# Kernel optimization log

Measured on AMD Instinct MI355X. Metric: run time of the kernel, lower is better.

## Reference

```python
import jax, jax.numpy as jnp
import numpy as np

H, HKV, D, HIDDEN = 32, 8, 128, 4096
G = H // HKV  # GQA group size = 4
ROPE_THETA = 10000.0


def fwht(x):
    """Fast Walsh-Hadamard transform over the last axis (scale=1, like faster_hadamard_transform default)."""
    d = x.shape[-1]
    orig = x.shape
    x = x.reshape(-1, d)
    h = 1
    while h < d:
        x = x.reshape(-1, d // (2 * h), 2, h)
        a, b = x[:, :, 0, :], x[:, :, 1, :]
        x = jnp.stack([a + b, a - b], axis=2).reshape(-1, d)
        h *= 2
    return x.reshape(orig)


def rope(x, pos):
    """NeoX-style (rotate-half) RoPE at scalar position `pos`; x: [..., D]."""
    half = D // 2
    inv_freq = 1.0 / (ROPE_THETA ** (jnp.arange(0, D, 2, dtype=jnp.float32) / D))  # [half]
    ang = jnp.float32(pos) * inv_freq
    cos, sin = jnp.cos(ang), jnp.sin(ang)
    x1, x2 = x[..., :half], x[..., half:]
    return jnp.concatenate([x1 * cos - x2 * sin, x2 * cos + x1 * sin], axis=-1)


def quant2bit(x):
    """2-bit quantization of Hadamard-domain vectors: per-vector scale = mean(|x|), codes in {-2,-1,0,1}."""
    s = jnp.mean(jnp.abs(x), axis=-1, keepdims=True) + 1e-6
    code = jnp.clip(jnp.round(x / s), -2.0, 1.0)
    return code, s


def _forward(hidden_states, Wq, Wk, Wv, Wo, k_cache, v_cache, top_k):
    x = hidden_states[0, 0]                                 # [HIDDEN]
    q = (x @ Wq.T).reshape(H, D)
    k = (x @ Wk.T).reshape(HKV, D)
    v = (x @ Wv.T).reshape(HKV, D)
    pos = k_cache.shape[0]                                  # decode position (cache len before append)
    q = rope(q, pos)
    k = rope(k, pos)
    # append to cache -> total T = S + 1 tokens
    K = jnp.concatenate([k_cache, k[None]], axis=0)          # [T, HKV, D]
    V = jnp.concatenate([v_cache, v[None]], axis=0)          # [T, HKV, D]
    T = K.shape[0]
    # Hadamard transform + 2-bit codes for estimation
    hq = fwht(q)                                             # [H, D]
    hK = fwht(K)                                             # [T, HKV, D]
    cq, sq = quant2bit(hq)                                   # [H,D], [H,1]
    ck, sk = quant2bit(hK)                                   # [T,HKV,D], [T,HKV,1]
    # estimated attention scores from low-bit codes, per query head
    est = jnp.einsum('ngd,tnd->ngt', cq.reshape(HKV, G, D), ck).reshape(H, T)
    skh = jnp.repeat(sk[:, :, 0].T, G, axis=0)               # [H, T]
    est = est * sq * skh
    est = est.at[:, -1].set(jnp.inf)                         # always keep the current token
    # top-k index selection per head
    _, idx = jax.lax.top_k(est, top_k)                       # [H, top_k]
    kv_map = jnp.arange(H) // G                              # [H]
    Ksel = K[idx, kv_map[:, None], :]                        # [H, top_k, D]
    Vsel = V[idx, kv_map[:, None], :]                        # [H, top_k, D]
    # sparse attention over selected tokens
    logits = jnp.einsum('hd,hkd->hk', q, Ksel) / jnp.sqrt(jnp.float32(D))
    p = jax.nn.softmax(logits, axis=-1)
    attn = jnp.einsum('hk,hkd->hd', p, Vsel).reshape(HIDDEN)
    return (attn @ Wo.T).reshape(1, 1, HIDDEN)


def setup_inputs() -> dict:
    key = jax.random.key(0)
    ks = jax.random.split(key, 7)
    S = 32767
    w = 1.0 / np.sqrt(HIDDEN)
    return {
        'hidden_states': jax.random.normal(ks[0], (1, 1, HIDDEN), jnp.float32),
        'Wq': jax.random.normal(ks[1], (H * D, HIDDEN), jnp.float32) * w,
        'Wk': jax.random.normal(ks[2], (HKV * D, HIDDEN), jnp.float32) * w,
        'Wv': jax.random.normal(ks[3], (HKV * D, HIDDEN), jnp.float32) * w,
        'Wo': jax.random.normal(ks[4], (HIDDEN, HIDDEN), jnp.float32) * w,
        'k_cache': jax.random.normal(ks[5], (S, HKV, D), jnp.float32),
        'v_cache': jax.random.normal(ks[6], (S, HKV, D), jnp.float32),
        'top_k': 2048,
    }


def reference(hidden_states, Wq, Wk, Wv, Wo, k_cache, v_cache, top_k):
    return _forward(hidden_states, Wq, Wk, Wv, Wo, k_cache, v_cache, top_k)
```

## Files before the change

kernel.cpp:

```cpp
#include <hip/hip_runtime.h>
#include <math.h>


#if defined(__has_builtin)
#if __has_builtin(__builtin_amdgcn_sdot4)
#define HAVE_SDOT4 1
#endif
#endif

__device__ __forceinline__ int dot4(int a, int b, int c) {
#ifdef HAVE_SDOT4
  return __builtin_amdgcn_sdot4(a, b, c, false);
#else
  return c + ((a << 24) >> 24) * ((b << 24) >> 24) +
         (((a << 16) >> 24)) * (((b << 16) >> 24)) +
         (((a << 8) >> 24)) * (((b << 8) >> 24)) + (a >> 24) * (b >> 24);
#endif
}

__device__ __forceinline__ unsigned enc_f32(float f) {
  unsigned u = __float_as_uint(f);
  return (u & 0x80000000u) ? ~u : (u | 0x80000000u);
}

__global__ __launch_bounds__(256) void k_gemv_qkv(
    const float* __restrict__ x, const float* __restrict__ Wq,
    const float* __restrict__ Wk, const float* __restrict__ Wv,
    float* __restrict__ y, unsigned* __restrict__ gz) {
  if (blockIdx.x < 96) {
    const int base = blockIdx.x * 512 + threadIdx.x;
    ((uint4*)gz)[base] = make_uint4(0u, 0u, 0u, 0u);
    ((uint4*)gz)[base + 256] = make_uint4(0u, 0u, 0u, 0u);
  }
  const int lane = threadIdx.x & 63;
  const int wid = threadIdx.x >> 6;
  const int row = blockIdx.x * 4 + wid;
  const float* W;
  if (row < 4096) W = Wq + (size_t)row * 4096;
  else if (row < 5120) W = Wk + (size_t)(row - 4096) * 4096;
  else W = Wv + (size_t)(row - 5120) * 4096;
  const float4* W4 = (const float4*)W;
  const float4* x4 = (const float4*)x;
  float acc = 0.f;
#pragma unroll
  for (int i = 0; i < 16; ++i) {
    float4 w = W4[i * 64 + lane];
    float4 xv = x4[i * 64 + lane];
    acc = fmaf(w.x, xv.x, acc);
    acc = fmaf(w.y, xv.y, acc);
    acc = fmaf(w.z, xv.z, acc);
    acc = fmaf(w.w, xv.w, acc);
  }
#pragma unroll
  for (int off = 32; off >= 1; off >>= 1) acc += __shfl_xor(acc, off);
  if (lane == 0) y[row] = acc;
}

__global__ __launch_bounds__(64) void k_rope_quant(
    const float* __restrict__ y, float* __restrict__ q_rope,
    float* __restrict__ k_rope, signed char* __restrict__ cq_i8,
    float* __restrict__ sq, int pos) {
  const int h = blockIdx.x;
  const int lane = threadIdx.x;
  const float* row = (h < 32) ? (y + (size_t)h * 128)
                              : (y + 4096 + (size_t)(h - 32) * 128);
  float x1 = row[lane];
  float x2 = row[lane + 64];
  double e = (double)lane / 64.0;
  float pf = (float)pow(10000.0, e);
  float invf = 1.0f / pf;
  float ang = (float)pos * invf;
  float c = (float)cos((double)ang);
  float s = (float)sin((double)ang);
  float r1 = __fsub_rn(__fmul_rn(x1, c), __fmul_rn(x2, s));
  float r2 = __fadd_rn(__fmul_rn(x2, c), __fmul_rn(x1, s));
  if (h >= 32) {
    k_rope[(size_t)(h - 32) * 128 + lane] = r1;
    k_rope[(size_t)(h - 32) * 128 + 64 + lane] = r2;
    return;
  }
  q_rope[(size_t)h * 128 + lane] = r1;
  q_rope[(size_t)h * 128 + 64 + lane] = r2;
  float a = r1, b = r2;
#pragma unroll
  for (int m = 1; m <= 32; m <<= 1) {
    float ta = __shfl_xor(a, m), tb = __shfl_xor(b, m);
    bool up = (lane & m) == 0;
    a = up ? (a + ta) : (ta - a);
    b = up ? (b + tb) : (tb - b);
  }
  { float na = a + b, nb = a - b; a = na; b = nb; }
  float asum = fabsf(a) + fabsf(b);
#pragma unroll
  for (int m = 32; m >= 1; m >>= 1) asum += __shfl_xor(asum, m);
  float sc = asum * (1.0f / 128.0f) + 1e-6f;
  float ca = fminf(fmaxf(rintf(a / sc), -2.0f), 1.0f);
  float cb = fminf(fmaxf(rintf(b / sc), -2.0f), 1.0f);
  cq_i8[(size_t)h * 128 + lane] = (signed char)(int)ca;
  cq_i8[(size_t)h * 128 + 64 + lane] = (signed char)(int)cb;
  if (lane == 0) sq[h] = sc;
}

__global__ __launch_bounds__(64, 1) void k_quant_est(
    const float* __restrict__ kc, const signed char* __restrict__ cq_i8,
    const float* __restrict__ sq, unsigned* __restrict__ ekeys, int S, int T) {
  const int lane = threadIdx.x;
  const int n = blockIdx.y;
  const int t = blockIdx.x * 64 + lane;
  const bool act = t < S;
  const float4* src = (const float4*)(kc + ((size_t)(act ? t : 0) * 8 + n) * 128);
  float f[128];
#pragma unroll
  for (int j = 0; j < 32; ++j) {
    float4 v = src[j];
    f[4 * j + 0] = v.x; f[4 * j + 1] = v.y; f[4 * j + 2] = v.z; f[4 * j + 3] = v.w;
  }
#pragma unroll
  for (int hh = 1; hh < 128; hh <<= 1) {
#pragma unroll
    for (int i = 0; i < 128; i += 2 * hh) {
#pragma unroll
      for (int k = 0; k < hh; ++k) {
        float a = f[i + k], b = f[i + hh + k];
        f[i + k] = a + b;
        f[i + hh + k] = a - b;
      }
    }
  }
  float s0 = 0.f, s1 = 0.f, s2 = 0.f, s3 = 0.f;
#pragma unroll
  for (int j = 0; j < 32; ++j) {
    s0 += fabsf(f[4 * j + 0]); s1 += fabsf(f[4 * j + 1]);
    s2 += fabsf(f[4 * j + 2]); s3 += fabsf(f[4 * j + 3]);
  }
  const float sc = ((s0 + s1) + (s2 + s3)) * (1.0f / 128.0f) + 1e-6f;
  unsigned pw[32];
#pragma unroll
  for (int w = 0; w < 32; ++w) {
    unsigned word = 0;
#pragma unroll
    for (int j = 0; j < 4; ++j) {
      float cf = fminf(fmaxf(rintf(f[4 * w + j] / sc), -2.0f), 1.0f);
      int ci = (int)cf;
      word |= ((unsigned)(ci & 255)) << (8 * j);
    }
    pw[w] = word;
  }
  int acc0 = 0, acc1 = 0, acc2 = 0, acc3 = 0;
  const int* cqw = (const int*)cq_i8;
#pragma unroll
  for (int w = 0; w < 32; ++w) {
    int ck = (int)pw[w];
    acc0 = dot4(ck, cqw[(n * 4 + 0) * 32 + w], acc0);
    acc1 = dot4(ck, cqw[(n * 4 + 1) * 32 + w], acc1);
    acc2 = dot4(ck, cqw[(n * 4 + 2) * 32 + w], acc2);
    acc3 = dot4(ck, cqw[(n * 4 + 3) * 32 + w], acc3);
  }
  int accs[4] = {acc0, acc1, acc2, acc3};
#pragma unroll
  for (int g = 0; g < 4; ++g) {
    float v = ((float)accs[g] * sq[n * 4 + g]) * sc;
    unsigned key = act ? enc_f32(v) : 0xFF800000u;
    ekeys[(size_t)(n * 4 + g) * T + t] = key;
  }
}

template <int NB>
__device__ __forceinline__ void radix_scan(const unsigned* __restrict__ hrow,
                                           unsigned need_in, unsigned& bsel,
                                           unsigned& need_out) {
  const int lane = threadIdx.x & 63;
  constexpr int PL = NB / 64;
  unsigned b[PL];
  unsigned s = 0u;
  const uint4* bp = (const uint4*)(hrow + lane * PL);
#pragma unroll
  for (int i = 0; i < PL / 4; ++i) {
    uint4 v = bp[i];
    b[4 * i] = v.x; b[4 * i + 1] = v.y; b[4 * i + 2] = v.z; b[4 * i + 3] = v.w;
    s += v.x + v.y + v.z + v.w;
  }
  unsigned inc = s;
#pragma unroll
  for (int off = 1; off < 64; off <<= 1) {
    unsigned tv = __shfl_down(inc, off);
    if (lane + off < 64) inc += tv;
  }
  const unsigned suf = inc - s;
  const bool win = (suf < need_in) && (suf + s >= need_in);
  unsigned bs = 0u, n2 = 0u;
  if (win) {
    unsigned running = suf;
#pragma unroll
    for (int i = PL - 1; i >= 0; --i) {
      unsigned cb = b[i];
      if (running + cb >= need_in) { bs = (unsigned)(lane * PL + i); n2 = need_in - running; break; }
      running += cb;
    }
  }
  unsigned long long mw = __ballot(win);
  int srcl = (int)__builtin_ctzll(mw);
  bsel = __shfl(bs, srcl);
  need_out = __shfl(n2, srcl);
}

__global__ __launch_bounds__(256) void k_hist(
    const unsigned* __restrict__ keys, const unsigned* __restrict__ g0,
    const unsigned* __restrict__ g1, unsigned* __restrict__ gout,
    const int* __restrict__ topk_ptr, int pass, int T) {
  const int h = blockIdx.y, c = blockIdx.x, tid = threadIdx.x;
  __shared__ unsigned lh[2048];
#pragma unroll
  for (int i = 0; i < 8; ++i) lh[tid + 256 * i] = 0u;

  int shift, pshift; unsigned mask;
  if (pass == 0) { shift = 21; mask = 0x7FFu; pshift = 0; }
  else if (pass == 1) { shift = 10; mask = 0x7FFu; pshift = 21; }
  else { shift = 0; mask = 0x3FFu; pshift = 10; }

  unsigned pref = 0u;
  if (pass >= 1) {
    const unsigned K = (unsigned)(*topk_ptr);
    unsigned b, nd;
    radix_scan<2048>(g0 + h * 2048, K, b, nd);
    pref = b;
    if (pass == 2) {
      unsigned b1, n1;
      radix_scan<2048>(g1 + h * 2048, nd, b1, n1);
      pref = (pref << 11) | b1;
    }
  }
  __syncthreads();
  const uint4* row = (const uint4*)(keys + (size_t)h * T + c * 2048);
#pragma unroll
  for (int j = 0; j < 2; ++j) {
    uint4 v = row[tid * 2 + j];
    unsigned u[4] = {v.x, v.y, v.z, v.w};
#pragma unroll
    for (int e = 0; e < 4; ++e) {
      bool ok = (pass == 0) || ((u[e] >> pshift) == pref);
      if (ok) atomicAdd(&lh[(u[e] >> shift) & mask], 1u);
    }
  }
  __syncthreads();
#pragma unroll
  for (int i = 0; i < 8; ++i) {
    unsigned cnt = lh[tid + 256 * i];
    if (cnt) atomicAdd(&gout[h * 2048 + tid + 256 * i], cnt);
  }
}

__global__ __launch_bounds__(256) void k_compact(
    const unsigned* __restrict__ keys, const unsigned* __restrict__ g0,
    const unsigned* __restrict__ g1, const unsigned* __restrict__ g2,
    int* __restrict__ idx_out, const int* __restrict__ topk_ptr, int T) {
  const int h = blockIdx.y, c = blockIdx.x, tid = threadIdx.x;
  const unsigned K = (unsigned)(*topk_ptr);
  unsigned b, need, thr;
  radix_scan<2048>(g0 + h * 2048, K, b, need);
  thr = b;
  radix_scan<2048>(g1 + h * 2048, need, b, need);
  thr = (thr << 11) | b;
  radix_scan<1024>(g2 + h * 2048, need, b, need);
  thr = (thr << 10) | b;
  const unsigned gt_total = K - need;

  const unsigned* rowbase = keys + (size_t)h * T;
  unsigned cg = 0u, ce = 0u;
  for (int i = 0; i < c; ++i) {
    const uint4* ch = (const uint4*)(rowbase + i * 2048);
#pragma unroll
    for (int j = 0; j < 2; ++j) {
      uint4 v = ch[tid * 2 + j];
      cg += (v.x > thr) + (v.y > thr) + (v.z > thr) + (v.w > thr);
      ce += (v.x == thr) + (v.y == thr) + (v.z == thr) + (v.w == thr);
    }
  }
  unsigned red = (cg << 16) | ce;
#pragma unroll
  for (int off = 32; off >= 1; off >>= 1) red += __shfl_xor(red, off);
  __shared__ unsigned wsum[4];
  __shared__ unsigned scn[256];
  if ((tid & 63) == 0) wsum[tid >> 6] = red;
  __syncthreads();
  const unsigned basep = wsum[0] + wsum[1] + wsum[2] + wsum[3];
  const unsigned bg = basep >> 16, be = basep & 0xFFFFu;

  const uint4* row = (const uint4*)(rowbase + c * 2048);
  unsigned u[8];
  {
    uint4 v0 = row[tid * 2], v1 = row[tid * 2 + 1];
    u[0] = v0.x; u[1] = v0.y; u[2] = v0.z; u[3] = v0.w;
    u[4] = v1.x; u[5] = v1.y; u[6] = v1.z; u[7] = v1.w;
  }
  unsigned mcg = 0u, mce = 0u;
#pragma unroll
  for (int e = 0; e < 8; ++e) { mcg += (u[e] > thr); mce += (u[e] == thr); }
  unsigned packed = (mcg << 16) | mce;
  scn[tid] = packed;
  __syncthreads();
#pragma unroll
  for (int off = 1; off < 256; off <<= 1) {
    unsigned v = (tid >= off) ? scn[tid - off] : 0u;
    __syncthreads();
    scn[tid] += v;
    __syncthreads();
  }
  const unsigned excl = scn[tid] - packed;
  unsigned exg = bg + (excl >> 16);
  unsigned exe = be + (excl & 0xFFFFu);
  const unsigned tb = (unsigned)(c * 2048 + tid * 8);
  int* dst = idx_out + (size_t)h * K;
#pragma unroll
  for (int e = 0; e < 8; ++e) {
    if (u[e] > thr) dst[exg++] = (int)(tb + e);
    else if (u[e] == thr) {
      unsigned r = exe++;
      if (r < need) dst[gt_total + r] = (int)(tb + e);
    }
  }
}

#define SPLITS 64
#define PSTR 132
__global__ __launch_bounds__(256) void k_attn(
    const float* __restrict__ kc, const float* __restrict__ vc,
    const float* __restrict__ k_rope, const float* __restrict__ v_new,
    const float* __restrict__ q_rope, const int* __restrict__ idx,
    const int* __restrict__ topk_ptr, float* __restrict__ part, int S) {
  const int lane = threadIdx.x & 63;
  const int wid = threadIdx.x >> 6;
  const int h = blockIdx.x;
  const int split = blockIdx.y;
  const int K = *topk_ptr;
  const int n = h >> 2;
  const int per_block = (K + SPLITS - 1) / SPLITS;
  const int j0 = split * per_block;
  const int j1 = min(K, j0 + per_block);
  const int per_wave = (per_block + 3) >> 2;
  const int base = j0 + wid * per_wave;
  float2 qv = ((const float2*)(q_rope + (size_t)h * 128))[lane];
  float ssum = 0.f, a0 = 0.f, a1 = 0.f;
  const float scl = 0.08838834764831845f;
  for (int b = 0; b < per_wave; b += 4) {
    float2 kk[4], vv[4];
    bool val[4];
#pragma unroll
    for (int u = 0; u < 4; ++u) {
      const int j = base + b + u;
      val[u] = (j < j1) && (base + b + u >= j0);
      int t = val[u] ? idx[(size_t)h * (size_t)K + j] : 0;
      const float* kr = (t < S) ? (kc + ((size_t)t * 8 + n) * 128)
                                : (k_rope + (size_t)n * 128);
      const float* vr = (t < S) ? (vc + ((size_t)t * 8 + n) * 128)
                                : (v_new + (size_t)n * 128);
      kk[u] = ((const float2*)kr)[lane];
      vv[u] = ((const float2*)vr)[lane];
    }
    float d[4];
#pragma unroll
    for (int u = 0; u < 4; ++u) d[u] = fmaf(qv.x, kk[u].x, qv.y * kk[u].y);
#pragma unroll
    for (int mm = 32; mm >= 1; mm >>= 1) {
#pragma unroll
      for (int u = 0; u < 4; ++u) d[u] += __shfl_xor(d[u], mm);
    }
#pragma unroll
    for (int u = 0; u < 4; ++u) {
      float p = val[u] ? expf(d[u] * scl) : 0.f;
      ssum += p;
      a0 = fmaf(p, vv[u].x, a0);
      a1 = fmaf(p, vv[u].y, a1);
    }
  }
  __shared__ float lds[4][129];
  lds[wid][2 * lane] = a0;
  lds[wid][2 * lane + 1] = a1;
  if (lane == 0) lds[wid][128] = ssum;
  __syncthreads();
  float* pp = part + (size_t)(h * SPLITS + split) * PSTR;
  const int tid = threadIdx.x;
  if (tid < 128) {
    float s = lds[0][tid] + lds[1][tid] + lds[2][tid] + lds[3][tid];
    pp[1 + tid] = s;
  } else if (tid == 128) {
    pp[0] = lds[0][128] + lds[1][128] + lds[2][128] + lds[3][128];
  }
}

__global__ __launch_bounds__(128) void k_combine(const float* __restrict__ part,
                                                 float* __restrict__ attn) {
  const int h = blockIdx.x;
  const int tid = threadIdx.x;
  const float* base = part + (size_t)h * SPLITS * PSTR;
  float acc = 0.f, ssum = 0.f;
  for (int s = 0; s < SPLITS; ++s) {
    const float* pp = base + (size_t)s * PSTR;
    acc += pp[1 + tid];
    ssum += pp[0];
  }
  attn[(size_t)h * 128 + tid] = acc / ssum;
}

__global__ __launch_bounds__(256) void k_gemv_out(
    const float* __restrict__ attn, const float* __restrict__ Wo,
    float* __restrict__ out) {
  const int lane = threadIdx.x & 63;
  const int wid = threadIdx.x >> 6;
  const int row = blockIdx.x * 4 + wid;
  const float4* W4 = (const float4*)(Wo + (size_t)row * 4096);
  const float4* x4 = (const float4*)attn;
  float acc = 0.f;
#pragma unroll
  for (int i = 0; i < 16; ++i) {
    float4 w = W4[i * 64 + lane];
    float4 xv = x4[i * 64 + lane];
    acc = fmaf(w.x, xv.x, acc);
    acc = fmaf(w.y, xv.y, acc);
    acc = fmaf(w.z, xv.z, acc);
    acc = fmaf(w.w, xv.w, acc);
  }
#pragma unroll
  for (int off = 32; off >= 1; off >>= 1) acc += __shfl_xor(acc, off);
  if (lane == 0) out[row] = acc;
}

extern "C" void kernel_launch(void* const* d_in, const int* in_sizes, int n_in,
                              void* d_out, int out_size, void* d_ws, size_t ws_size,
                              hipStream_t stream) {
  const float* x  = (const float*)d_in[0];
  const float* Wq = (const float*)d_in[1];
  const float* Wk = (const float*)d_in[2];
  const float* Wv = (const float*)d_in[3];
  const float* Wo = (const float*)d_in[4];
  const float* kc = (const float*)d_in[5];
  const float* vc = (const float*)d_in[6];
  const int* topk_ptr = (const int*)d_in[7];
  const int S = in_sizes[5] / (8 * 128);
  const int T = S + 1;

  float* ws = (float*)d_ws;
  float* y      = ws + 0;
  float* q_rope = ws + 6144;
  float* k_rope = ws + 10240;
  float* sq     = ws + 11264;
  float* attn   = ws + 11328;
  signed char* cq_i8 = (signed char*)(ws + 15424);
  unsigned* ekeys = (unsigned*)(ws + 16448);
  unsigned* ghist = (unsigned*)(ws + 1065024);
  unsigned* g0 = ghist, *g1 = ghist + 65536, *g2 = ghist + 131072;
  int*   idx    = (int*)(ws + 1261632);
  float* part   = ws + 1523776;

  const int chunks = T / 2048;

  k_gemv_qkv<<<1536, 256, 0, stream>>>(x, Wq, Wk, Wv, y, ghist);
  k_rope_quant<<<40, 64, 0, stream>>>(y, q_rope, k_rope, cq_i8, sq, S);
  k_quant_est<<<dim3(T / 64, 8), 64, 0, stream>>>(kc, cq_i8, sq, ekeys, S, T);

  k_hist<<<dim3(chunks, 32), 256, 0, stream>>>(ekeys, g0, g1, g0, topk_ptr, 0, T);
  k_hist<<<dim3(chunks, 32), 256, 0, stream>>>(ekeys, g0, g1, g1, topk_ptr, 1, T);
  k_hist<<<dim3(chunks, 32), 256, 0, stream>>>(ekeys, g0, g1, g2, topk_ptr, 2, T);
  k_compact<<<dim3(chunks, 32), 256, 0, stream>>>(ekeys, g0, g1, g2, idx, topk_ptr, T);

  k_attn<<<dim3(32, SPLITS), 256, 0, stream>>>(kc, vc, k_rope, y + 5120, q_rope,
                                               idx, topk_ptr, part, S);
  k_combine<<<32, 128, 0, stream>>>(part, attn);
  k_gemv_out<<<1024, 256, 0, stream>>>(attn, Wo, (float*)d_out);
}
```

Before: 116.9 us.

## Stage K-cache rows through swizzled LDS tile for coalesced loads in quant_est

The quantize-and-estimate kernel used to have each lane read its own 512-byte K row with strided float4 loads. Each 64-lane block now loads a contiguous 32KB slab (64 rows covering 8 tokens by 8 KV heads) with fully coalesced float4 reads. It stores the slab into shared memory with a rotation swizzle to avoid bank conflicts, and each lane then reads its row from LDS. The grid is flattened so each lane's head and token come from the lane index, and a bounds guard is added on the key writes. The cost is 32KB of LDS per block, which may limit occupancy, plus an extra sync and LDS round-trip; the ekeys writes also become more scattered across heads.

```diff
diff --git a/kernel.cpp b/kernel.cpp
--- a/kernel.cpp
+++ b/kernel.cpp
@@ -104,15 +104,27 @@
 __global__ __launch_bounds__(64, 1) void k_quant_est(
     const float* __restrict__ kc, const signed char* __restrict__ cq_i8,
     const float* __restrict__ sq, unsigned* __restrict__ ekeys, int S, int T) {
-  const int lane = threadIdx.x;
-  const int n = blockIdx.y;
-  const int t = blockIdx.x * 64 + lane;
-  const bool act = t < S;
-  const float4* src = (const float4*)(kc + ((size_t)(act ? t : 0) * 8 + n) * 128);
+  __shared__ float tile[8192];
+  const int l = threadIdx.x;
+  const int R = S * 8;
+  const size_t base4 = (size_t)blockIdx.x * 2048;
+  const float4* kc4 = (const float4*)kc;
+  float4* tile4 = (float4*)tile;
+#pragma unroll
+  for (int i = 0; i < 32; ++i) {
+    const int F = i * 64 + l;
+    const int row = F >> 5;
+    const int c = F & 31;
+    const long gr = (long)blockIdx.x * 64 + row;
+    const size_t gidx = (gr < R) ? (base4 + (size_t)F) : (size_t)c;
+    float4 v = kc4[gidx];
+    tile4[row * 32 + ((c + row) & 31)] = v;
+  }
+  __syncthreads();
   float f[128];
 #pragma unroll
   for (int j = 0; j < 32; ++j) {
-    float4 v = src[j];
+    float4 v = tile4[l * 32 + ((j + l) & 31)];
     f[4 * j + 0] = v.x; f[4 * j + 1] = v.y; f[4 * j + 2] = v.z; f[4 * j + 3] = v.w;
   }
 #pragma unroll
@@ -146,6 +158,7 @@
     }
     pw[w] = word;
   }
+  const int n = l & 7;
   int acc0 = 0, acc1 = 0, acc2 = 0, acc3 = 0;
   const int* cqw = (const int*)cq_i8;
 #pragma unroll
@@ -156,12 +169,16 @@
     acc2 = dot4(ck, cqw[(n * 4 + 2) * 32 + w], acc2);
     acc3 = dot4(ck, cqw[(n * 4 + 3) * 32 + w], acc3);
   }
+  const int t = blockIdx.x * 8 + (l >> 3);
+  const bool act = t < S;
   int accs[4] = {acc0, acc1, acc2, acc3};
-#pragma unroll
-  for (int g = 0; g < 4; ++g) {
-    float v = ((float)accs[g] * sq[n * 4 + g]) * sc;
-    unsigned key = act ? enc_f32(v) : 0xFF800000u;
-    ekeys[(size_t)(n * 4 + g) * T + t] = key;
+  if (t < T) {
+#pragma unroll
+    for (int g = 0; g < 4; ++g) {
+      float v = ((float)accs[g] * sq[n * 4 + g]) * sc;
+      unsigned key = act ? enc_f32(v) : 0xFF800000u;
+      ekeys[(size_t)(n * 4 + g) * T + t] = key;
+    }
   }
 }
 
@@ -453,10 +470,11 @@
   float* part   = ws + 1523776;
 
   const int chunks = T / 2048;
+  const int nblk = (8 * S + 8 + 63) / 64;
 
   k_gemv_qkv<<<1536, 256, 0, stream>>>(x, Wq, Wk, Wv, y, ghist);
   k_rope_quant<<<40, 64, 0, stream>>>(y, q_rope, k_rope, cq_i8, sq, S);
-  k_quant_est<<<dim3(T / 64, 8), 64, 0, stream>>>(kc, cq_i8, sq, ekeys, S, T);
+  k_quant_est<<<nblk, 64, 0, stream>>>(kc, cq_i8, sq, ekeys, S, T);
 
   k_hist<<<dim3(chunks, 32), 256, 0, stream>>>(ekeys, g0, g1, g0, topk_ptr, 0, T);
   k_hist<<<dim3(chunks, 32), 256, 0, stream>>>(ekeys, g0, g1, g1, topk_ptr, 1, T);
```

Result: slower. 141.6 us (+21.2%).

## Remap quant-estimate threads to contiguous cache rows and vectorize Hadamard butterflies

Applied to the files above, without the earlier changes.

The quant/estimate kernel now assigns one thread per flattened (token, kv-head) row, so each 64-thread block reads one contiguous stretch of the K cache instead of rows strided across heads. The 128-point Walsh-Hadamard transform is rewritten as explicit float4-vector butterflies. Quantization is fused directly into the int8 dot-product loop, removing the packed-code array and easing register pressure. In exchange, score-key writes become less coalesced, because neighbouring lanes now write to eight different head rows.

```diff
diff --git a/kernel.cpp b/kernel.cpp
--- a/kernel.cpp
+++ b/kernel.cpp
@@ -1,6 +1,8 @@
 #include <hip/hip_runtime.h>
 #include <math.h>
 
+
+typedef __attribute__((ext_vector_type(4))) float f32x4;
 
 #if defined(__has_builtin)
 #if __has_builtin(__builtin_amdgcn_sdot4)
@@ -101,67 +103,78 @@
   if (lane == 0) sq[h] = sc;
 }
 
+#define REP32(M) M(0) M(1) M(2) M(3) M(4) M(5) M(6) M(7) M(8) M(9) M(10) M(11) \
+  M(12) M(13) M(14) M(15) M(16) M(17) M(18) M(19) M(20) M(21) M(22) M(23) \
+  M(24) M(25) M(26) M(27) M(28) M(29) M(30) M(31)
+
 __global__ __launch_bounds__(64, 1) void k_quant_est(
     const float* __restrict__ kc, const signed char* __restrict__ cq_i8,
     const float* __restrict__ sq, unsigned* __restrict__ ekeys, int S, int T) {
   const int lane = threadIdx.x;
-  const int n = blockIdx.y;
-  const int t = blockIdx.x * 64 + lane;
-  const bool act = t < S;
-  const float4* src = (const float4*)(kc + ((size_t)(act ? t : 0) * 8 + n) * 128);
-  float f[128];
-#pragma unroll
-  for (int j = 0; j < 32; ++j) {
-    float4 v = src[j];
-    f[4 * j + 0] = v.x; f[4 * j + 1] = v.y; f[4 * j + 2] = v.z; f[4 * j + 3] = v.w;
-  }
-#pragma unroll
-  for (int hh = 1; hh < 128; hh <<= 1) {
-#pragma unroll
-    for (int i = 0; i < 128; i += 2 * hh) {
-#pragma unroll
-      for (int k = 0; k < hh; ++k) {
-        float a = f[i + k], b = f[i + hh + k];
-        f[i + k] = a + b;
-        f[i + hh + k] = a - b;
-      }
-    }
-  }
-  float s0 = 0.f, s1 = 0.f, s2 = 0.f, s3 = 0.f;
-#pragma unroll
-  for (int j = 0; j < 32; ++j) {
-    s0 += fabsf(f[4 * j + 0]); s1 += fabsf(f[4 * j + 1]);
-    s2 += fabsf(f[4 * j + 2]); s3 += fabsf(f[4 * j + 3]);
-  }
-  const float sc = ((s0 + s1) + (s2 + s3)) * (1.0f / 128.0f) + 1e-6f;
-  unsigned pw[32];
-#pragma unroll
-  for (int w = 0; w < 32; ++w) {
-    unsigned word = 0;
-#pragma unroll
-    for (int j = 0; j < 4; ++j) {
-      float cf = fminf(fmaxf(rintf(f[4 * w + j] / sc), -2.0f), 1.0f);
-      int ci = (int)cf;
-      word |= ((unsigned)(ci & 255)) << (8 * j);
-    }
-    pw[w] = word;
-  }
+  const int R = S * 8;
+  const long r = (long)blockIdx.x * 64 + lane;
+  const bool act = r < R;
+  const f32x4* src = (const f32x4*)(kc + (act ? r : 0) * 128);
+
+#define DECL(i) f32x4 F##i = src[i];
+  REP32(DECL)
+#undef DECL
+
+#define S1(i) { f32x4 t = F##i; F##i = (f32x4){t.x + t.y, t.x - t.y, t.z + t.w, t.z - t.w}; }
+  REP32(S1)
+#undef S1
+#define S2(i) { f32x4 t = F##i; F##i = (f32x4){t.x + t.z, t.y + t.w, t.x - t.z, t.y - t.w}; }
+  REP32(S2)
+#undef S2
+#define BF(i, j) { f32x4 t = F##i; F##i = t + F##j; F##j = t - F##j; }
+  BF(0,1) BF(2,3) BF(4,5) BF(6,7) BF(8,9) BF(10,11) BF(12,13) BF(14,15)
+  BF(16,17) BF(18,19) BF(20,21) BF(22,23) BF(24,25) BF(26,27) BF(28,29) BF(30,31)
+  BF(0,2) BF(1,3) BF(4,6) BF(5,7) BF(8,10) BF(9,11) BF(12,14) BF(13,15)
+  BF(16,18) BF(17,19) BF(20,22) BF(21,23) BF(24,26) BF(25,27) BF(28,30) BF(29,31)
+  BF(0,4) BF(1,5) BF(2,6) BF(3,7) BF(8,12) BF(9,13) BF(10,14) BF(11,15)
+  BF(16,20) BF(17,21) BF(18,22) BF(19,23) BF(24,28) BF(25,29) BF(26,30) BF(27,31)
+  BF(0,8) BF(1,9) BF(2,10) BF(3,11) BF(4,12) BF(5,13) BF(6,14) BF(7,15)
+  BF(16,24) BF(17,25) BF(18,26) BF(19,27) BF(20,28) BF(21,29) BF(22,30) BF(23,31)
+  BF(0,16) BF(1,17) BF(2,18) BF(3,19) BF(4,20) BF(5,21) BF(6,22) BF(7,23)
+  BF(8,24) BF(9,25) BF(10,26) BF(11,27) BF(12,28) BF(13,29) BF(14,30) BF(15,31)
+#undef BF
+
+  f32x4 sv = (f32x4){0.f, 0.f, 0.f, 0.f};
+#define FA(i) sv += (f32x4){fabsf(F##i.x), fabsf(F##i.y), fabsf(F##i.z), fabsf(F##i.w)};
+  REP32(FA)
+#undef FA
+  const float sc = ((sv.x + sv.y) + (sv.z + sv.w)) * (1.0f / 128.0f) + 1e-6f;
+
+  const int n = (int)(r & 7);
+  const int* cqw = (const int*)cq_i8;
+  const int* cqn0 = cqw + (n * 4 + 0) * 32;
+  const int* cqn1 = cqw + (n * 4 + 1) * 32;
+  const int* cqn2 = cqw + (n * 4 + 2) * 32;
+  const int* cqn3 = cqw + (n * 4 + 3) * 32;
   int acc0 = 0, acc1 = 0, acc2 = 0, acc3 = 0;
-  const int* cqw = (const int*)cq_i8;
-#pragma unroll
-  for (int w = 0; w < 32; ++w) {
-    int ck = (int)pw[w];
-    acc0 = dot4(ck, cqw[(n * 4 + 0) * 32 + w], acc0);
-    acc1 = dot4(ck, cqw[(n * 4 + 1) * 32 + w], acc1);
-    acc2 = dot4(ck, cqw[(n * 4 + 2) * 32 + w], acc2);
-    acc3 = dot4(ck, cqw[(n * 4 + 3) * 32 + w], acc3);
-  }
+#define QD(i) { \
+    int c0 = (int)fminf(fmaxf(rintf(F##i.x / sc), -2.0f), 1.0f); \
+    int c1 = (int)fminf(fmaxf(rintf(F##i.y / sc), -2.0f), 1.0f); \
+    int c2 = (int)fminf(fmaxf(rintf(F##i.z / sc), -2.0f), 1.0f); \
+    int c3 = (int)fminf(fmaxf(rintf(F##i.w / sc), -2.0f), 1.0f); \
+    int word = (c0 & 255) | ((c1 & 255) << 8) | ((c2 & 255) << 16) | ((c3 & 255) << 24); \
+    acc0 = dot4(word, cqn0[i], acc0); \
+    acc1 = dot4(word, cqn1[i], acc1); \
+    acc2 = dot4(word, cqn2[i], acc2); \
+    acc3 = dot4(word, cqn3[i], acc3); }
+  REP32(QD)
+#undef QD
+
+  const int t = (int)(r >> 3);
+  const bool live = (int)(r >> 3) < S;
   int accs[4] = {acc0, acc1, acc2, acc3};
-#pragma unroll
-  for (int g = 0; g < 4; ++g) {
-    float v = ((float)accs[g] * sq[n * 4 + g]) * sc;
-    unsigned key = act ? enc_f32(v) : 0xFF800000u;
-    ekeys[(size_t)(n * 4 + g) * T + t] = key;
+  if (t < T) {
+#pragma unroll
+    for (int g = 0; g < 4; ++g) {
+      float v = ((float)accs[g] * sq[n * 4 + g]) * sc;
+      unsigned key = live ? enc_f32(v) : 0xFF800000u;
+      ekeys[(size_t)(n * 4 + g) * T + t] = key;
+    }
   }
 }
 
@@ -453,10 +466,11 @@
   float* part   = ws + 1523776;
 
   const int chunks = T / 2048;
+  const int nblk = (8 * S + 8) / 64;
 
   k_gemv_qkv<<<1536, 256, 0, stream>>>(x, Wq, Wk, Wv, y, ghist);
   k_rope_quant<<<40, 64, 0, stream>>>(y, q_rope, k_rope, cq_i8, sq, S);
-  k_quant_est<<<dim3(T / 64, 8), 64, 0, stream>>>(kc, cq_i8, sq, ekeys, S, T);
+  k_quant_est<<<nblk, 64, 0, stream>>>(kc, cq_i8, sq, ekeys, S, T);
 
   k_hist<<<dim3(chunks, 32), 256, 0, stream>>>(ekeys, g0, g1, g0, topk_ptr, 0, T);
   k_hist<<<dim3(chunks, 32), 256, 0, stream>>>(ekeys, g0, g1, g1, topk_ptr, 1, T);
```

New measurement: 148.0 us. 1.27x slower.
